# Optimization experiments

Measured on AMD Instinct MI355X. Metric: run time of the kernel, lower is better.

Reference implementation:

```python
import jax, jax.numpy as jnp
import numpy as np

# Block-diagonal SplitMLP: fc1 group g sees [day | items[g]]; fc2 is purely per-group.
B, C, V, H, O, G = 128, 16, 32, 64, 4, 10000


def setup_inputs() -> dict:
    key = jax.random.key(0)
    ks = jax.random.split(key, 7)
    bound1 = 1.0 / np.sqrt(C + V * G)   # nn.Linear init bound for fc1 (full fan-in)
    bound2 = 1.0 / np.sqrt(H * G)       # fc2 fan-in
    return {
        "day": jax.random.normal(ks[0], (B, C), jnp.float32),
        "items": jax.random.normal(ks[1], (B, G, V), jnp.float32),
        "W1_day": jax.random.uniform(ks[2], (G, H, C), jnp.float32, -bound1, bound1),
        "W1_var": jax.random.uniform(ks[3], (G, H, V), jnp.float32, -bound1, bound1),
        "b1": jax.random.uniform(ks[4], (G, H), jnp.float32, -bound1, bound1),
        "W2": jax.random.uniform(ks[5], (G, O, H), jnp.float32, -bound2, bound2),
        "b2": jax.random.uniform(ks[6], (G, O), jnp.float32, -bound2, bound2),
    }


def reference(day, items, W1_day, W1_var, b1, W2, b2):
    # fc1: shared day columns + per-group var block, then ReLU
    h = (
        jnp.einsum("bc,ghc->bgh", day, W1_day)
        + jnp.einsum("bgv,ghv->bgh", items, W1_var)
        + b1
    )
    h = jax.nn.relu(h)
    # fc2: purely block-diagonal (num_const = 0)
    y = jnp.einsum("bgh,goh->bgo", h, W2) + b2  # (B, G, O)
    return y
```

## Files before the change

### kernel.cpp

```cpp
#include <hip/hip_runtime.h>
#include <hip/hip_bf16.h>


typedef __bf16 v8bf __attribute__((ext_vector_type(8)));
typedef __bf16 v4bf __attribute__((ext_vector_type(4)));
typedef float  v4f  __attribute__((ext_vector_type(4)));

#define B_  128
#define C_  16
#define V_  32
#define H_  64
#define O_  4
#define G_  10000
#define AK  72

__device__ __forceinline__ v4bf cvt4(float4 f) {
  v4bf r;
  r[0] = (__bf16)f.x; r[1] = (__bf16)f.y; r[2] = (__bf16)f.z; r[3] = (__bf16)f.w;
  return r;
}

__global__ __launch_bounds__(256, 3)
void splitmlp_kernel(const float* __restrict__ day,
                     const float* __restrict__ items,
                     const float* __restrict__ W1d,
                     const float* __restrict__ W1v,
                     const float* __restrict__ b1,
                     const float* __restrict__ W2,
                     const float* __restrict__ b2,
                     float* __restrict__ out) {
  __shared__ alignas(16) __bf16 Abuf[B_ * AK];
  __shared__ alignas(16) __bf16 Wbuf[H_ * AK];
  __shared__ alignas(16) __bf16 Hbuf[B_ * AK];
  __shared__ alignas(16) __bf16 W2buf[16 * H_];
  __shared__ float b1s[H_];
  __shared__ float b2s[O_];

  const int t = threadIdx.x;
  const int g = blockIdx.x;

  __bf16 zb = (__bf16)0.0f;
  v4bf z4 = {zb, zb, zb, zb};

  {
    const float4* p = reinterpret_cast<const float4*>(day);
#pragma unroll
    for (int i = t; i < 512; i += 256) {
      int b = i >> 2, c4 = (i & 3) << 2;
      *reinterpret_cast<v4bf*>(&Abuf[b * AK + c4]) = cvt4(p[i]);
    }
  }
  {
#pragma unroll
    for (int i = t; i < 1024; i += 256) {
      int b = i >> 3, v4i = (i & 7) << 2;
      const float4* p = reinterpret_cast<const float4*>(
          items + (size_t)b * (G_ * V_) + (size_t)g * V_ + v4i);
      *reinterpret_cast<v4bf*>(&Abuf[b * AK + C_ + v4i]) = cvt4(*p);
    }
  }
  {
#pragma unroll
    for (int i = t; i < 512; i += 256) {
      int b = i >> 2, c4 = 48 + ((i & 3) << 2);
      *reinterpret_cast<v4bf*>(&Abuf[b * AK + c4]) = z4;
    }
  }
  {
    const float4* p = reinterpret_cast<const float4*>(W1d + (size_t)g * (H_ * C_));
    int h = t >> 2, c4 = (t & 3) << 2;
    *reinterpret_cast<v4bf*>(&Wbuf[h * AK + c4]) = cvt4(p[t]);
  }
  {
    const float4* p = reinterpret_cast<const float4*>(W1v + (size_t)g * (H_ * V_));
#pragma unroll
    for (int i = t; i < 512; i += 256) {
      int h = i >> 3, v4i = (i & 7) << 2;
      *reinterpret_cast<v4bf*>(&Wbuf[h * AK + C_ + v4i]) = cvt4(p[i]);
    }
  }
  {
    int h = t >> 2, c4 = 48 + ((t & 3) << 2);
    *reinterpret_cast<v4bf*>(&Wbuf[h * AK + c4]) = z4;
  }
  if (t < 64) {
    const float4* p = reinterpret_cast<const float4*>(W2 + (size_t)g * (O_ * H_));
    int o = t >> 4, h4 = (t & 15) << 2;
    *reinterpret_cast<v4bf*>(&W2buf[o * H_ + h4]) = cvt4(p[t]);
  }
  if (t < 192) {
    int o = 4 + (t >> 4), h4 = (t & 15) << 2;
    *reinterpret_cast<v4bf*>(&W2buf[o * H_ + h4]) = z4;
  }
  if (t < H_) b1s[t] = b1[(size_t)g * H_ + t];
  if (t < O_) b2s[t] = b2[(size_t)g * O_ + t];

  __syncthreads();

  const int w = t >> 6;
  const int lane = t & 63;
  const int c = lane & 15;
  const int q = lane >> 4;
  const int rowA0 = w * 32 + c;
  const int rowA1 = rowA0 + 16;

  v4f zero = {0.f, 0.f, 0.f, 0.f};
  v4f acc[2][4];
#pragma unroll
  for (int m = 0; m < 2; ++m)
#pragma unroll
    for (int n = 0; n < 4; ++n) acc[m][n] = zero;

#pragma unroll
  for (int kt = 0; kt < 2; ++kt) {
    int k0 = kt * 32 + q * 8;
    v8bf a0 = *reinterpret_cast<const v8bf*>(&Abuf[rowA0 * AK + k0]);
    v8bf a1 = *reinterpret_cast<const v8bf*>(&Abuf[rowA1 * AK + k0]);
#pragma unroll
    for (int n = 0; n < 4; ++n) {
      v8bf bw = *reinterpret_cast<const v8bf*>(&Wbuf[(n * 16 + c) * AK + k0]);
      acc[0][n] = __builtin_amdgcn_mfma_f32_16x16x32_bf16(a0, bw, acc[0][n], 0, 0, 0);
      acc[1][n] = __builtin_amdgcn_mfma_f32_16x16x32_bf16(a1, bw, acc[1][n], 0, 0, 0);
    }
  }

#pragma unroll
  for (int n = 0; n < 4; ++n) {
    float bias = b1s[n * 16 + c];
#pragma unroll
    for (int m = 0; m < 2; ++m) {
      int rb = w * 32 + m * 16 + q * 4;
#pragma unroll
      for (int r = 0; r < 4; ++r) {
        float v = acc[m][n][r] + bias;
        v = fmaxf(v, 0.0f);
        Hbuf[(rb + r) * AK + n * 16 + c] = (__bf16)v;
      }
    }
  }

  v4f y0 = zero, y1 = zero;
#pragma unroll
  for (int kt = 0; kt < 2; ++kt) {
    int k0 = kt * 32 + q * 8;
    v8bf h0  = *reinterpret_cast<const v8bf*>(&Hbuf[rowA0 * AK + k0]);
    v8bf h1  = *reinterpret_cast<const v8bf*>(&Hbuf[rowA1 * AK + k0]);
    v8bf w2f = *reinterpret_cast<const v8bf*>(&W2buf[c * H_ + k0]);
    y0 = __builtin_amdgcn_mfma_f32_16x16x32_bf16(h0, w2f, y0, 0, 0, 0);
    y1 = __builtin_amdgcn_mfma_f32_16x16x32_bf16(h1, w2f, y1, 0, 0, 0);
  }

  if (c < O_) {
    float bb = b2s[c];
#pragma unroll
    for (int m = 0; m < 2; ++m) {
      int rb = w * 32 + m * 16 + q * 4;
      v4f ym = (m == 0) ? y0 : y1;
#pragma unroll
      for (int r = 0; r < 4; ++r) {
        out[(size_t)(rb + r) * (G_ * O_) + (size_t)g * O_ + c] = ym[r] + bb;
      }
    }
  }
}

extern "C" void kernel_launch(void* const* d_in, const int* in_sizes, int n_in,
                              void* d_out, int out_size, void* d_ws, size_t ws_size,
                              hipStream_t stream) {
  const float* day   = (const float*)d_in[0];
  const float* items = (const float*)d_in[1];
  const float* W1d   = (const float*)d_in[2];
  const float* W1v   = (const float*)d_in[3];
  const float* b1    = (const float*)d_in[4];
  const float* W2    = (const float*)d_in[5];
  const float* b2    = (const float*)d_in[6];
  float* out = (float*)d_out;
  splitmlp_kernel<<<G_, 256, 0, stream>>>(day, items, W1d, W1v, b1, W2, b2, out);
}
```

Measured before the change: 369.6 us.

## Load MFMA operands directly from global memory, drop LDS staging and barrier

Removes the shared-memory staging of the fc1 activations and weights. Each lane now loads its MFMA fragments straight from global memory and converts them to bf16 in registers, which drops the __syncthreads barrier. The fc2 MFMA operands are swapped so each row's four outputs sit together and can be written as one float4 store. With far less LDS per block, launch bounds rise to target 6 blocks per CU. The cost is redundant, partly uncoalesced global reads of the weights across waves, and it relies on caches to absorb them.

Measured after the change: 395.2 us. 6.9% more time.

```diff
diff --git a/kernel.cpp b/kernel.cpp
--- a/kernel.cpp
+++ b/kernel.cpp
@@ -3,7 +3,6 @@
 
 
 typedef __bf16 v8bf __attribute__((ext_vector_type(8)));
-typedef __bf16 v4bf __attribute__((ext_vector_type(4)));
 typedef float  v4f  __attribute__((ext_vector_type(4)));
 
 #define B_  128
@@ -12,15 +11,23 @@
 #define H_  64
 #define O_  4
 #define G_  10000
-#define AK  72
+#define HS  104
 
-__device__ __forceinline__ v4bf cvt4(float4 f) {
-  v4bf r;
-  r[0] = (__bf16)f.x; r[1] = (__bf16)f.y; r[2] = (__bf16)f.z; r[3] = (__bf16)f.w;
+__device__ __forceinline__ v8bf cvt8(float4 lo, float4 hi) {
+  v8bf r;
+  r[0] = (__bf16)lo.x; r[1] = (__bf16)lo.y; r[2] = (__bf16)lo.z; r[3] = (__bf16)lo.w;
+  r[4] = (__bf16)hi.x; r[5] = (__bf16)hi.y; r[6] = (__bf16)hi.z; r[7] = (__bf16)hi.w;
   return r;
 }
 
-__global__ __launch_bounds__(256, 3)
+__device__ __forceinline__ v8bf gload8(const float* __restrict__ p) {
+  const float4* p4 = reinterpret_cast<const float4*>(p);
+  float4 lo = p4[0];
+  float4 hi = p4[1];
+  return cvt8(lo, hi);
+}
+
+__global__ __launch_bounds__(256, 6)
 void splitmlp_kernel(const float* __restrict__ day,
                      const float* __restrict__ items,
                      const float* __restrict__ W1d,
@@ -29,82 +36,31 @@
                      const float* __restrict__ W2,
                      const float* __restrict__ b2,
                      float* __restrict__ out) {
-  __shared__ alignas(16) __bf16 Abuf[B_ * AK];
-  __shared__ alignas(16) __bf16 Wbuf[H_ * AK];
-  __shared__ alignas(16) __bf16 Hbuf[B_ * AK];
-  __shared__ alignas(16) __bf16 W2buf[16 * H_];
-  __shared__ float b1s[H_];
-  __shared__ float b2s[O_];
+  __shared__ __bf16 Hbuf[B_ * HS];
 
-  const int t = threadIdx.x;
-  const int g = blockIdx.x;
+  const int t    = threadIdx.x;
+  const int g    = blockIdx.x;
+  const int w    = t >> 6;
+  const int lane = t & 63;
+  const int c    = lane & 15;
+  const int q    = lane >> 4;
+  const int r0   = w * 32;
+  const int bA0  = r0 + c;
+  const int bA1  = bA0 + 16;
 
-  __bf16 zb = (__bf16)0.0f;
-  v4bf z4 = {zb, zb, zb, zb};
+  const size_t gV   = (size_t)g * V_;
+  const float* W1dg = W1d + (size_t)g * (H_ * C_);
+  const float* W1vg = W1v + (size_t)g * (H_ * V_);
 
-  {
-    const float4* p = reinterpret_cast<const float4*>(day);
+  v8bf zf;
 #pragma unroll
-    for (int i = t; i < 512; i += 256) {
-      int b = i >> 2, c4 = (i & 3) << 2;
-      *reinterpret_cast<v4bf*>(&Abuf[b * AK + c4]) = cvt4(p[i]);
-    }
-  }
-  {
+  for (int i = 0; i < 8; ++i) zf[i] = (__bf16)0.0f;
+  v4f zero = {0.f, 0.f, 0.f, 0.f};
+
+  float bias[4];
 #pragma unroll
-    for (int i = t; i < 1024; i += 256) {
-      int b = i >> 3, v4i = (i & 7) << 2;
-      const float4* p = reinterpret_cast<const float4*>(
-          items + (size_t)b * (G_ * V_) + (size_t)g * V_ + v4i);
-      *reinterpret_cast<v4bf*>(&Abuf[b * AK + C_ + v4i]) = cvt4(*p);
-    }
-  }
-  {
-#pragma unroll
-    for (int i = t; i < 512; i += 256) {
-      int b = i >> 2, c4 = 48 + ((i & 3) << 2);
-      *reinterpret_cast<v4bf*>(&Abuf[b * AK + c4]) = z4;
-    }
-  }
-  {
-    const float4* p = reinterpret_cast<const float4*>(W1d + (size_t)g * (H_ * C_));
-    int h = t >> 2, c4 = (t & 3) << 2;
-    *reinterpret_cast<v4bf*>(&Wbuf[h * AK + c4]) = cvt4(p[t]);
-  }
-  {
-    const float4* p = reinterpret_cast<const float4*>(W1v + (size_t)g * (H_ * V_));
-#pragma unroll
-    for (int i = t; i < 512; i += 256) {
-      int h = i >> 3, v4i = (i & 7) << 2;
-      *reinterpret_cast<v4bf*>(&Wbuf[h * AK + C_ + v4i]) = cvt4(p[i]);
-    }
-  }
-  {
-    int h = t >> 2, c4 = 48 + ((t & 3) << 2);
-    *reinterpret_cast<v4bf*>(&Wbuf[h * AK + c4]) = z4;
-  }
-  if (t < 64) {
-    const float4* p = reinterpret_cast<const float4*>(W2 + (size_t)g * (O_ * H_));
-    int o = t >> 4, h4 = (t & 15) << 2;
-    *reinterpret_cast<v4bf*>(&W2buf[o * H_ + h4]) = cvt4(p[t]);
-  }
-  if (t < 192) {
-    int o = 4 + (t >> 4), h4 = (t & 15) << 2;
-    *reinterpret_cast<v4bf*>(&W2buf[o * H_ + h4]) = z4;
-  }
-  if (t < H_) b1s[t] = b1[(size_t)g * H_ + t];
-  if (t < O_) b2s[t] = b2[(size_t)g * O_ + t];
+  for (int n = 0; n < 4; ++n) bias[n] = b1[(size_t)g * H_ + n * 16 + c];
 
-  __syncthreads();
-
-  const int w = t >> 6;
-  const int lane = t & 63;
-  const int c = lane & 15;
-  const int q = lane >> 4;
-  const int rowA0 = w * 32 + c;
-  const int rowA1 = rowA0 + 16;
-
-  v4f zero = {0.f, 0.f, 0.f, 0.f};
   v4f acc[2][4];
 #pragma unroll
   for (int m = 0; m < 2; ++m)
@@ -113,54 +69,62 @@
 
 #pragma unroll
   for (int kt = 0; kt < 2; ++kt) {
-    int k0 = kt * 32 + q * 8;
-    v8bf a0 = *reinterpret_cast<const v8bf*>(&Abuf[rowA0 * AK + k0]);
-    v8bf a1 = *reinterpret_cast<const v8bf*>(&Abuf[rowA1 * AK + k0]);
+    const int  k0    = kt * 32 + q * 8;
+    const bool isday = (k0 < 16);
+    const bool valid = (k0 < 48);
+
+    const float* pa0 = isday ? (day + bA0 * C_ + k0)
+                     : valid ? (items + (size_t)bA0 * (G_ * V_) + gV + (k0 - 16))
+                             : day;
+    const float* pa1 = isday ? (day + bA1 * C_ + k0)
+                     : valid ? (items + (size_t)bA1 * (G_ * V_) + gV + (k0 - 16))
+                             : day;
+    v8bf a0 = gload8(pa0);
+    v8bf a1 = gload8(pa1);
+    if (!valid) { a0 = zf; a1 = zf; }
+
 #pragma unroll
     for (int n = 0; n < 4; ++n) {
-      v8bf bw = *reinterpret_cast<const v8bf*>(&Wbuf[(n * 16 + c) * AK + k0]);
+      const int h = n * 16 + c;
+      const float* pw = isday ? (W1dg + h * C_ + k0)
+                      : valid ? (W1vg + h * V_ + (k0 - 16))
+                              : day;
+      v8bf bw = gload8(pw);
       acc[0][n] = __builtin_amdgcn_mfma_f32_16x16x32_bf16(a0, bw, acc[0][n], 0, 0, 0);
       acc[1][n] = __builtin_amdgcn_mfma_f32_16x16x32_bf16(a1, bw, acc[1][n], 0, 0, 0);
     }
   }
 
 #pragma unroll
-  for (int n = 0; n < 4; ++n) {
-    float bias = b1s[n * 16 + c];
+  for (int n = 0; n < 4; ++n)
 #pragma unroll
-    for (int m = 0; m < 2; ++m) {
-      int rb = w * 32 + m * 16 + q * 4;
+    for (int m = 0; m < 2; ++m)
 #pragma unroll
       for (int r = 0; r < 4; ++r) {
-        float v = acc[m][n][r] + bias;
-        v = fmaxf(v, 0.0f);
-        Hbuf[(rb + r) * AK + n * 16 + c] = (__bf16)v;
+        float v = fmaxf(acc[m][n][r] + bias[n], 0.0f);
+        Hbuf[(r0 + m * 16 + q * 4 + r) * HS + n * 16 + c] = (__bf16)v;
       }
-    }
-  }
 
   v4f y0 = zero, y1 = zero;
 #pragma unroll
   for (int kt = 0; kt < 2; ++kt) {
-    int k0 = kt * 32 + q * 8;
-    v8bf h0  = *reinterpret_cast<const v8bf*>(&Hbuf[rowA0 * AK + k0]);
-    v8bf h1  = *reinterpret_cast<const v8bf*>(&Hbuf[rowA1 * AK + k0]);
-    v8bf w2f = *reinterpret_cast<const v8bf*>(&W2buf[c * H_ + k0]);
-    y0 = __builtin_amdgcn_mfma_f32_16x16x32_bf16(h0, w2f, y0, 0, 0, 0);
-    y1 = __builtin_amdgcn_mfma_f32_16x16x32_bf16(h1, w2f, y1, 0, 0, 0);
+    const int k0 = kt * 32 + q * 8;
+    const float* pw2 = (c < O_) ? (W2 + (size_t)g * (O_ * H_) + c * H_ + k0) : day;
+    v8bf wf = gload8(pw2);
+    if (c >= O_) wf = zf;
+    v8bf h0 = *reinterpret_cast<const v8bf*>(&Hbuf[(r0 + c) * HS + k0]);
+    v8bf h1 = *reinterpret_cast<const v8bf*>(&Hbuf[(r0 + 16 + c) * HS + k0]);
+    y0 = __builtin_amdgcn_mfma_f32_16x16x32_bf16(wf, h0, y0, 0, 0, 0);
+    y1 = __builtin_amdgcn_mfma_f32_16x16x32_bf16(wf, h1, y1, 0, 0, 0);
   }
 
-  if (c < O_) {
-    float bb = b2s[c];
-#pragma unroll
-    for (int m = 0; m < 2; ++m) {
-      int rb = w * 32 + m * 16 + q * 4;
-      v4f ym = (m == 0) ? y0 : y1;
-#pragma unroll
-      for (int r = 0; r < 4; ++r) {
-        out[(size_t)(rb + r) * (G_ * O_) + (size_t)g * O_ + c] = ym[r] + bb;
-      }
-    }
+  if (q == 0) {
+    const float4 b2v = *reinterpret_cast<const float4*>(b2 + (size_t)g * O_);
+    float4 o0, o1;
+    o0.x = y0[0] + b2v.x; o0.y = y0[1] + b2v.y; o0.z = y0[2] + b2v.z; o0.w = y0[3] + b2v.w;
+    o1.x = y1[0] + b2v.x; o1.y = y1[1] + b2v.y; o1.z = y1[2] + b2v.z; o1.w = y1[3] + b2v.w;
+    *reinterpret_cast<float4*>(out + (size_t)(r0 + c) * (G_ * O_) + (size_t)g * O_) = o0;
+    *reinterpret_cast<float4*>(out + (size_t)(r0 + 16 + c) * (G_ * O_) + (size_t)g * O_) = o1;
   }
 }
 
```
